# Performance work log

Hardware: AMD Instinct MI355X
Metric: run time of the kernel (lower is better)

Reference implementation:

```python
import jax, jax.numpy as jnp
import numpy as np

B, CL, H, W, NP = 128, 8, 16, 16, 32   # batch, primary cap length, height, width, n primary capsules
NC, CLO, ITER = 10, 16, 3              # n output capsules, output capsule length, routing iterations


def squash(t):
    # TensorMONK Activations 'squash': squash along axis 2 of a 3D tensor
    ss = jnp.sum(t * t, axis=2, keepdims=True)
    return (ss / (1.0 + ss)) * t / jnp.sqrt(ss)


def setup_inputs() -> dict:
    key = jax.random.key(0)
    k1, k2 = jax.random.split(key)
    tensor = jax.random.normal(k1, (B, CL, H, W, NP), dtype=jnp.float32)
    # nn.Parameter(torch.randn(...).normal_(0.0, 0.1)) -> N(0, 0.1)
    weight = 0.1 * jax.random.normal(k2, (CL * H * W, NP, NC * CLO), dtype=jnp.float32)
    return {"tensor": tensor, "weight": weight}


def reference(tensor, weight):
    b, cl, h, w, n_prim = tensor.shape
    # flatten spatial/length dims, squash along primary-capsule axis (dim 2, faithful to source)
    x = squash(tensor.reshape(b, -1, n_prim))                  # (B, P, N) with P = cl*h*w
    # (B,P,1,N) @ (P,N,K) broadcasted matmul -> (B,P,K)
    u = jnp.einsum('bpn,pnk->bpk', x, weight)
    u = u.reshape(b, cl, h, w, NC, CLO)                        # (B, cl, h, w, NC, CLO)
    bias = jnp.zeros((b, cl, h, w, NC), dtype=tensor.dtype)
    v = None
    for i in range(ITER):  # fixed small iteration count
        c = jax.nn.softmax(bias, axis=4)                       # softmax over output capsules
        s = jnp.einsum('bchwn,bchwnk->bnk', c, u)              # weighted sum over cl,h,w
        v = squash(s)                                          # squash along capsule length (axis 2)
        if i < ITER - 1:
            bias = bias + jnp.einsum('bchwnk,bnk->bchwn', u, v)
    return v
```

## Files before the change

kernel.cpp:

```cpp
#include <hip/hip_runtime.h>

typedef unsigned short u16;
typedef __attribute__((ext_vector_type(8))) short bf16x8;
typedef __attribute__((ext_vector_type(4))) float f32x4;

#define B_   128
#define P_   2048
#define NC_  10
#define F_   160
#define NBLK 512
#define PPB  4
#define NTHR 512
#define XS   40
#define WS   40

__device__ __forceinline__ u16 f2bf(float f) {
    union { float f; unsigned u; } v; v.f = f;
    unsigned r = v.u + 0x7FFFu + ((v.u >> 16) & 1u);
    return (u16)(r >> 16);
}
__device__ __forceinline__ float bf2f(u16 h) {
    union { unsigned u; float f; } v; v.u = ((unsigned)h) << 16;
    return v.f;
}

__global__ void k_squash_x(const float* __restrict__ t, u16* __restrict__ xb) {
    int g = blockIdx.x * 256 + threadIdx.x;
    int pair = g >> 2, sub = g & 3;
    int p = pair & 2047, b = pair >> 11;
    const float4* tg = (const float4*)t;
    int fi = pair * 8 + sub * 2;
    float4 va = tg[fi], vb = tg[fi + 1];
    float ss = va.x*va.x + va.y*va.y + va.z*va.z + va.w*va.w
             + vb.x*vb.x + vb.y*vb.y + vb.z*vb.z + vb.w*vb.w;
    ss += __shfl_xor(ss, 1);
    ss += __shfl_xor(ss, 2);
    float fct = ss / ((1.f + ss) * sqrtf(ss));
    u16 h[8] __attribute__((aligned(16)));
    h[0]=f2bf(va.x*fct); h[1]=f2bf(va.y*fct); h[2]=f2bf(va.z*fct); h[3]=f2bf(va.w*fct);
    h[4]=f2bf(vb.x*fct); h[5]=f2bf(vb.y*fct); h[6]=f2bf(vb.z*fct); h[7]=f2bf(vb.w*fct);
    *(uint4*)(xb + (p * 128 + b) * 32 + sub * 8) = *(const uint4*)h;
}

__global__ void k_wt(const float* __restrict__ w, u16* __restrict__ wb) {
    __shared__ u16 wl[32 * F_];
    int p = blockIdx.x, tid = threadIdx.x;
    const float4* wp = (const float4*)(w + p * 32 * F_);
    for (int e4 = tid; e4 < 1280; e4 += 256) {
        float4 v = wp[e4];
        u16 h[4] __attribute__((aligned(8)));
        h[0]=f2bf(v.x); h[1]=f2bf(v.y); h[2]=f2bf(v.z); h[3]=f2bf(v.w);
        *(ushort4*)(wl + e4 * 4) = *(const ushort4*)h;
    }
    __syncthreads();
    u16* wo = wb + p * F_ * 32;
    for (int sid = tid; sid < 640; sid += 256) {
        int f = sid >> 2, k0 = (sid & 3) << 3;
        u16 tmp[8] __attribute__((aligned(16)));
#pragma unroll
        for (int j = 0; j < 8; ++j) tmp[j] = wl[(k0 + j) * F_ + f];
        *(uint4*)(wo + f * 32 + k0) = *(const uint4*)tmp;
    }
}

template<int MODE>
__global__ __launch_bounds__(NTHR, 2) void k_pass(
        const u16* __restrict__ xb, const u16* __restrict__ wb,
        const float* __restrict__ vprev, u16* __restrict__ s_part)
{
    __shared__ u16 xt[128 * XS];
    __shared__ u16 wt[F_ * WS];
    const int tid = threadIdx.x, blk = blockIdx.x;
    const int L = tid & 63, wv = tid >> 6;
    const int q = L >> 4, col = L & 15;
    const int b = wv * 16 + col;
    const int p0 = blk * PPB;

    float4 vv[NC_];
    if (MODE != 0) {
#pragma unroll
        for (int n = 0; n < NC_; ++n)
            vv[n] = *(const float4*)(vprev + b * F_ + n * 16 + q * 4);
    }

    f32x4 s_acc[NC_];
#pragma unroll
    for (int n = 0; n < NC_; ++n) s_acc[n] = (f32x4){0.f, 0.f, 0.f, 0.f};

    uint4 r0, r1, r2;
    {
        const uint4* xg = (const uint4*)(xb + p0 * 4096);
        const uint4* wg = (const uint4*)(wb + p0 * 5120);
        r0 = xg[tid]; r1 = wg[tid];
        if (tid < 128) r2 = wg[tid + 512];
    }

#pragma unroll
    for (int pp = 0; pp < PPB; ++pp) {
        __syncthreads();
        *(uint4*)&xt[(tid >> 2) * XS + (tid & 3) * 8] = r0;
        *(uint4*)&wt[(tid >> 2) * WS + (tid & 3) * 8] = r1;
        if (tid < 128)
            *(uint4*)&wt[(128 + (tid >> 2)) * WS + (tid & 3) * 8] = r2;
        if (pp + 1 < PPB) {
            const uint4* xg = (const uint4*)(xb + (p0 + pp + 1) * 4096);
            const uint4* wg = (const uint4*)(wb + (p0 + pp + 1) * 5120);
            r0 = xg[tid]; r1 = wg[tid];
            if (tid < 128) r2 = wg[tid + 512];
        }
        __syncthreads();

        bf16x8 bfrag = *(const bf16x8*)&xt[b * XS + q * 8];
        if (MODE == 0) {
#pragma unroll
            for (int n = 0; n < NC_; ++n) {
                bf16x8 afrag = *(const bf16x8*)&wt[(n * 16 + col) * WS + q * 8];
                s_acc[n] = __builtin_amdgcn_mfma_f32_16x16x32_bf16(afrag, bfrag, s_acc[n], 0, 0, 0);
            }
        } else {
            float tt[NC_];
#pragma unroll
            for (int n = 0; n < NC_; ++n) {
                bf16x8 afrag = *(const bf16x8*)&wt[(n * 16 + col) * WS + q * 8];
                f32x4 z = {0.f, 0.f, 0.f, 0.f};
                f32x4 acc = __builtin_amdgcn_mfma_f32_16x16x32_bf16(afrag, bfrag, z, 0, 0, 0);
                float t = acc[0]*vv[n].x + acc[1]*vv[n].y + acc[2]*vv[n].z + acc[3]*vv[n].w;
                t += __shfl_xor(t, 16);
                t += __shfl_xor(t, 32);
                tt[n] = t;
            }
            float mx = tt[0];
#pragma unroll
            for (int n = 1; n < NC_; ++n) mx = fmaxf(mx, tt[n]);
            float den = 0.f;
#pragma unroll
            for (int n = 0; n < NC_; ++n) { tt[n] = __expf(tt[n] - mx); den += tt[n]; }
            float inv = 1.f / den;
#pragma unroll
            for (int n = 0; n < NC_; ++n) {
                bf16x8 afrag = *(const bf16x8*)&wt[(n * 16 + col) * WS + q * 8];
                f32x4 z = {0.f, 0.f, 0.f, 0.f};
                f32x4 acc = __builtin_amdgcn_mfma_f32_16x16x32_bf16(afrag, bfrag, z, 0, 0, 0);
                float cf = tt[n] * inv;
#pragma unroll
                for (int r = 0; r < 4; ++r) s_acc[n][r] += cf * acc[r];
            }
        }
    }

    u16* sp = s_part + blk * (B_ * F_);
    const float sc = (MODE == 0) ? 0.1f : 1.f;
#pragma unroll
    for (int n = 0; n < NC_; ++n) {
        u16 h[4] __attribute__((aligned(8)));
#pragma unroll
        for (int r = 0; r < 4; ++r) h[r] = f2bf(s_acc[n][r] * sc);
        *(ushort4*)(sp + b * F_ + n * 16 + q * 4) = *(const ushort4*)h;
    }
}

template<int ADD>
__global__ void k_red(const u16* __restrict__ s_part,
                      const float* __restrict__ vprev, float* __restrict__ vout) {
    __shared__ float r0s[256], r1s[256];
    const int tid = threadIdx.x, blk = blockIdx.x;
    const int pid = tid & 31, part = tid >> 5;
    const uint* sp = (const uint*)s_part;
    const int opair = blk * 32 + pid;
    float a0 = 0.f, a1 = 0.f;
#pragma unroll 8
    for (int g = part; g < NBLK; g += 8) {
        uint u = sp[g * 10240 + opair];
        a0 += bf2f((u16)(u & 0xffff));
        a1 += bf2f((u16)(u >> 16));
    }
    r0s[tid] = a0; r1s[tid] = a1;
    __syncthreads();
    if (tid < 32) {
        float s0 = 0.f, s1 = 0.f;
#pragma unroll
        for (int k = 0; k < 8; ++k) { s0 += r0s[k * 32 + tid]; s1 += r1s[k * 32 + tid]; }
        float sq = s0 * s0 + s1 * s1;
        sq += __shfl_xor(sq, 1);
        sq += __shfl_xor(sq, 2);
        sq += __shfl_xor(sq, 4);
        float fct = sq / ((1.f + sq) * sqrtf(sq));
        float2 o = make_float2(s0 * fct, s1 * fct);
        if (ADD) {
            float2 pv = *(const float2*)(vprev + 2 * (blk * 32 + tid));
            o.x += pv.x; o.y += pv.y;
        }
        *(float2*)(vout + 2 * (blk * 32 + tid)) = o;
    }
}

extern "C" void kernel_launch(void* const* d_in, const int* in_sizes, int n_in,
                              void* d_out, int out_size, void* d_ws, size_t ws_size,
                              hipStream_t stream) {
    const float* tensor = (const float*)d_in[0];
    const float* weight = (const float*)d_in[1];
    float* out = (float*)d_out;
    char* ws = (char*)d_ws;

    u16*   xb     = (u16*)(ws);
    u16*   wb     = (u16*)(ws + 16777216);
    u16*   s_part = (u16*)(ws + 37748736);
    float* v0     = (float*)(ws + 58720256);
    float* vs     = (float*)(ws + 58802176);

    k_squash_x<<<4096, 256, 0, stream>>>(tensor, xb);
    k_wt<<<2048, 256, 0, stream>>>(weight, wb);

    k_pass<0><<<NBLK, NTHR, 0, stream>>>(xb, wb, nullptr, s_part);
    k_red<0><<<320, 256, 0, stream>>>(s_part, nullptr, v0);
    k_pass<1><<<NBLK, NTHR, 0, stream>>>(xb, wb, v0, s_part);
    k_red<1><<<320, 256, 0, stream>>>(s_part, v0, vs);
    k_pass<2><<<NBLK, NTHR, 0, stream>>>(xb, wb, vs, s_part);
    k_red<0><<<320, 256, 0, stream>>>(s_part, nullptr, out);
}
```

Baseline: 175.4 us.

## Use direct global-to-LDS loads with double buffering and swizzled layout; merge prep kernels

Replaces register-staged loads into padded shared memory with async global_load_lds into double-buffered LDS tiles. The padding is replaced by an XOR-style swizzle applied when the prep kernels write their outputs, which avoids bank conflicts without a padded stride. The two prep kernels are merged into one launch. This cuts LDS write instructions and one barrier per step, and overlaps the next tile's load with compute, at the cost of doubling LDS use per block.

```diff
diff --git a/kernel.cpp b/kernel.cpp
--- a/kernel.cpp
+++ b/kernel.cpp
@@ -1,4 +1,5 @@
 #include <hip/hip_runtime.h>
+#include <cstdint>
 
 typedef unsigned short u16;
 typedef __attribute__((ext_vector_type(8))) short bf16x8;
@@ -11,8 +12,6 @@
 #define NBLK 512
 #define PPB  4
 #define NTHR 512
-#define XS   40
-#define WS   40
 
 __device__ __forceinline__ u16 f2bf(float f) {
     union { float f; unsigned u; } v; v.f = f;
@@ -24,42 +23,53 @@
     return v.f;
 }
 
-__global__ void k_squash_x(const float* __restrict__ t, u16* __restrict__ xb) {
-    int g = blockIdx.x * 256 + threadIdx.x;
-    int pair = g >> 2, sub = g & 3;
-    int p = pair & 2047, b = pair >> 11;
-    const float4* tg = (const float4*)t;
-    int fi = pair * 8 + sub * 2;
-    float4 va = tg[fi], vb = tg[fi + 1];
-    float ss = va.x*va.x + va.y*va.y + va.z*va.z + va.w*va.w
-             + vb.x*vb.x + vb.y*vb.y + vb.z*vb.z + vb.w*vb.w;
-    ss += __shfl_xor(ss, 1);
-    ss += __shfl_xor(ss, 2);
-    float fct = ss / ((1.f + ss) * sqrtf(ss));
-    u16 h[8] __attribute__((aligned(16)));
-    h[0]=f2bf(va.x*fct); h[1]=f2bf(va.y*fct); h[2]=f2bf(va.z*fct); h[3]=f2bf(va.w*fct);
-    h[4]=f2bf(vb.x*fct); h[5]=f2bf(vb.y*fct); h[6]=f2bf(vb.z*fct); h[7]=f2bf(vb.w*fct);
-    *(uint4*)(xb + (p * 128 + b) * 32 + sub * 8) = *(const uint4*)h;
-}
-
-__global__ void k_wt(const float* __restrict__ w, u16* __restrict__ wb) {
-    __shared__ u16 wl[32 * F_];
-    int p = blockIdx.x, tid = threadIdx.x;
-    const float4* wp = (const float4*)(w + p * 32 * F_);
-    for (int e4 = tid; e4 < 1280; e4 += 256) {
-        float4 v = wp[e4];
-        u16 h[4] __attribute__((aligned(8)));
-        h[0]=f2bf(v.x); h[1]=f2bf(v.y); h[2]=f2bf(v.z); h[3]=f2bf(v.w);
-        *(ushort4*)(wl + e4 * 4) = *(const ushort4*)h;
-    }
-    __syncthreads();
-    u16* wo = wb + p * F_ * 32;
-    for (int sid = tid; sid < 640; sid += 256) {
-        int f = sid >> 2, k0 = (sid & 3) << 3;
-        u16 tmp[8] __attribute__((aligned(16)));
-#pragma unroll
-        for (int j = 0; j < 8; ++j) tmp[j] = wl[(k0 + j) * F_ + f];
-        *(uint4*)(wo + f * 32 + k0) = *(const uint4*)tmp;
+__device__ __forceinline__ void gl_lds16(const void* g, void* l) {
+    typedef __attribute__((address_space(3))) unsigned lds_uint;
+    typedef __attribute__((address_space(1))) const unsigned glob_uint;
+    __builtin_amdgcn_global_load_lds((glob_uint*)(uintptr_t)g,
+                                     (lds_uint*)(unsigned)(uintptr_t)l, 16, 0, 0);
+}
+
+__global__ void k_prep(const float* __restrict__ t, const float* __restrict__ w,
+                       u16* __restrict__ xb, u16* __restrict__ wb) {
+    const int blk = blockIdx.x, tid = threadIdx.x;
+    if (blk < 4096) {
+        int g = blk * 256 + tid;
+        int pair = g >> 2, sub = g & 3;
+        int p = pair & 2047, b = pair >> 11;
+        const float4* tg = (const float4*)t;
+        int fi = pair * 8 + sub * 2;
+        float4 va = tg[fi], vb = tg[fi + 1];
+        float ss = va.x*va.x + va.y*va.y + va.z*va.z + va.w*va.w
+                 + vb.x*vb.x + vb.y*vb.y + vb.z*vb.z + vb.w*vb.w;
+        ss += __shfl_xor(ss, 1);
+        ss += __shfl_xor(ss, 2);
+        float fct = ss / ((1.f + ss) * sqrtf(ss));
+        u16 h[8] __attribute__((aligned(16)));
+        h[0]=f2bf(va.x*fct); h[1]=f2bf(va.y*fct); h[2]=f2bf(va.z*fct); h[3]=f2bf(va.w*fct);
+        h[4]=f2bf(vb.x*fct); h[5]=f2bf(vb.y*fct); h[6]=f2bf(vb.z*fct); h[7]=f2bf(vb.w*fct);
+        int off = (sub + (b >> 1)) & 3;
+        *(uint4*)(xb + p * 4096 + b * 32 + off * 8) = *(const uint4*)h;
+    } else {
+        __shared__ u16 wl[32 * F_];
+        int p = blk - 4096;
+        const float4* wp = (const float4*)(w + p * 32 * F_);
+        for (int e4 = tid; e4 < 1280; e4 += 256) {
+            float4 v = wp[e4];
+            u16 h[4] __attribute__((aligned(8)));
+            h[0]=f2bf(v.x); h[1]=f2bf(v.y); h[2]=f2bf(v.z); h[3]=f2bf(v.w);
+            *(ushort4*)(wl + e4 * 4) = *(const ushort4*)h;
+        }
+        __syncthreads();
+        u16* wo = wb + p * 5120;
+        for (int sid = tid; sid < 640; sid += 256) {
+            int f = sid >> 2, k0 = (sid & 3) << 3, q = sid & 3;
+            u16 tmp[8] __attribute__((aligned(16)));
+#pragma unroll
+            for (int j = 0; j < 8; ++j) tmp[j] = wl[(k0 + j) * F_ + f];
+            int off = (q + (f >> 1)) & 3;
+            *(uint4*)(wo + f * 32 + off * 8) = *(const uint4*)tmp;
+        }
     }
 }
 
@@ -68,13 +78,14 @@
         const u16* __restrict__ xb, const u16* __restrict__ wb,
         const float* __restrict__ vprev, u16* __restrict__ s_part)
 {
-    __shared__ u16 xt[128 * XS];
-    __shared__ u16 wt[F_ * WS];
+    __shared__ __align__(16) u16 xt[2][4096];
+    __shared__ __align__(16) u16 wt[2][5120];
     const int tid = threadIdx.x, blk = blockIdx.x;
     const int L = tid & 63, wv = tid >> 6;
     const int q = L >> 4, col = L & 15;
     const int b = wv * 16 + col;
     const int p0 = blk * PPB;
+    const int off8 = ((q + (col >> 1)) & 3) * 8;
 
     float4 vv[NC_];
     if (MODE != 0) {
@@ -87,41 +98,36 @@
 #pragma unroll
     for (int n = 0; n < NC_; ++n) s_acc[n] = (f32x4){0.f, 0.f, 0.f, 0.f};
 
-    uint4 r0, r1, r2;
-    {
-        const uint4* xg = (const uint4*)(xb + p0 * 4096);
-        const uint4* wg = (const uint4*)(wb + p0 * 5120);
-        r0 = xg[tid]; r1 = wg[tid];
-        if (tid < 128) r2 = wg[tid + 512];
-    }
-
+    auto issue = [&](int p, int c) {
+        const u16* xg = xb + p * 4096 + wv * 512 + L * 8;
+        const u16* wg = wb + p * 5120 + wv * 512 + L * 8;
+        gl_lds16(xg, &xt[c][wv * 512]);
+        gl_lds16(wg, &wt[c][wv * 512]);
+        if (wv < 2)
+            gl_lds16(wb + p * 5120 + (8 + wv) * 512 + L * 8, &wt[c][(8 + wv) * 512]);
+    };
+
+    issue(p0, 0);
 #pragma unroll
     for (int pp = 0; pp < PPB; ++pp) {
+        __builtin_amdgcn_s_waitcnt(0x0f70);
         __syncthreads();
-        *(uint4*)&xt[(tid >> 2) * XS + (tid & 3) * 8] = r0;
-        *(uint4*)&wt[(tid >> 2) * WS + (tid & 3) * 8] = r1;
-        if (tid < 128)
-            *(uint4*)&wt[(128 + (tid >> 2)) * WS + (tid & 3) * 8] = r2;
-        if (pp + 1 < PPB) {
-            const uint4* xg = (const uint4*)(xb + (p0 + pp + 1) * 4096);
-            const uint4* wg = (const uint4*)(wb + (p0 + pp + 1) * 5120);
-            r0 = xg[tid]; r1 = wg[tid];
-            if (tid < 128) r2 = wg[tid + 512];
-        }
-        __syncthreads();
-
-        bf16x8 bfrag = *(const bf16x8*)&xt[b * XS + q * 8];
+        if (pp + 1 < PPB) issue(p0 + pp + 1, (pp + 1) & 1);
+        const u16* xc = xt[pp & 1];
+        const u16* wc = wt[pp & 1];
+
+        bf16x8 bfrag = *(const bf16x8*)&xc[b * 32 + off8];
         if (MODE == 0) {
 #pragma unroll
             for (int n = 0; n < NC_; ++n) {
-                bf16x8 afrag = *(const bf16x8*)&wt[(n * 16 + col) * WS + q * 8];
+                bf16x8 afrag = *(const bf16x8*)&wc[(n * 16 + col) * 32 + off8];
                 s_acc[n] = __builtin_amdgcn_mfma_f32_16x16x32_bf16(afrag, bfrag, s_acc[n], 0, 0, 0);
             }
         } else {
             float tt[NC_];
 #pragma unroll
             for (int n = 0; n < NC_; ++n) {
-                bf16x8 afrag = *(const bf16x8*)&wt[(n * 16 + col) * WS + q * 8];
+                bf16x8 afrag = *(const bf16x8*)&wc[(n * 16 + col) * 32 + off8];
                 f32x4 z = {0.f, 0.f, 0.f, 0.f};
                 f32x4 acc = __builtin_amdgcn_mfma_f32_16x16x32_bf16(afrag, bfrag, z, 0, 0, 0);
                 float t = acc[0]*vv[n].x + acc[1]*vv[n].y + acc[2]*vv[n].z + acc[3]*vv[n].w;
@@ -138,7 +144,7 @@
             float inv = 1.f / den;
 #pragma unroll
             for (int n = 0; n < NC_; ++n) {
-                bf16x8 afrag = *(const bf16x8*)&wt[(n * 16 + col) * WS + q * 8];
+                bf16x8 afrag = *(const bf16x8*)&wc[(n * 16 + col) * 32 + off8];
                 f32x4 z = {0.f, 0.f, 0.f, 0.f};
                 f32x4 acc = __builtin_amdgcn_mfma_f32_16x16x32_bf16(afrag, bfrag, z, 0, 0, 0);
                 float cf = tt[n] * inv;
@@ -208,8 +214,7 @@
     float* v0     = (float*)(ws + 58720256);
     float* vs     = (float*)(ws + 58802176);
 
-    k_squash_x<<<4096, 256, 0, stream>>>(tensor, xb);
-    k_wt<<<2048, 256, 0, stream>>>(weight, wb);
+    k_prep<<<6144, 256, 0, stream>>>(tensor, weight, xb, wb);
 
     k_pass<0><<<NBLK, NTHR, 0, stream>>>(xb, wb, nullptr, s_part);
     k_red<0><<<320, 256, 0, stream>>>(s_part, nullptr, v0);
```

Result: no change. 176.8 us (+0.8%).
